# Optimization experiments

Hardware: AMD Instinct MI355X
Metric: run time of the kernel (lower is better)

Reference implementation:

```python
import jax, jax.numpy as jnp
import numpy as np

BETA = 1.0  # lagr_softmax default inverse temperature

def setup_inputs() -> dict:
    key = jax.random.key(0)
    ks = jax.random.split(key, 5)
    B, Tq, Tk, Eq, Ek, E, H = 2, 2048, 2048, 1024, 1024, 1024, 16
    s = lambda d: 1.0 / np.sqrt(d)
    return {
        "gq": jax.random.normal(ks[0], (B, Tq, Eq), jnp.float32),
        "gk": jax.random.normal(ks[1], (B, Tk, Ek), jnp.float32),
        "WQ": jax.random.normal(ks[2], (E, Eq), jnp.float32) * s(Eq),
        "WK": jax.random.normal(ks[3], (E, Ek), jnp.float32) * s(Ek),
        "Wmix": jax.random.normal(ks[4], (1, H), jnp.float32) * s(H),
    }

def reference(gq, gk, WQ, WK, Wmix):
    B, Tq, _ = gq.shape
    H = Wmix.shape[1]
    E = WQ.shape[0]
    D = E // H
    # Linear projections (bias=False): x @ W.T
    q = (gq @ WQ.T).reshape(B, Tq, H, D)          # (B,Tq,H,D)
    k = (gk @ WK.T).reshape(B, -1, H, D)          # (B,Tk,H,D)
    # scores q @ k^T per head: (B,H,Tq,Tk)
    a = jnp.einsum('bqhd,bkhd->bhqk', q, k)
    # mix_heads: Linear(n_heads -> 1) applied over head axis
    a = jnp.einsum('bhqk,h->bqk', a, Wmix[0])     # (B,Tq,Tk)
    # lagr_softmax: (1/beta) * logsumexp(beta * a, dim=-1)
    out = jax.nn.logsumexp(BETA * a, axis=-1) / BETA  # (B,Tq)
    return out[:, None, :]                        # (B,1,Tq) matching torch shape
```

## Files before the change

kernel.cpp:

```cpp
#include <hip/hip_runtime.h>
#include <hip/hip_bf16.h>
#include <math.h>

#define B_    2
#define TQ    2048
#define TK    2048
#define E_    1024
#define MTOT  4096

typedef __attribute__((ext_vector_type(8))) short bf16x8;
typedef __attribute__((ext_vector_type(4))) float f32x4;

__device__ __forceinline__ unsigned short f2bf(float x) {
  unsigned int u = __float_as_uint(x);
  u += 0x7fff + ((u >> 16) & 1);
  return (unsigned short)(u >> 16);
}

__device__ __forceinline__ void load_lds16(const void* g, void* l) {
  __builtin_amdgcn_global_load_lds(
      (const __attribute__((address_space(1))) unsigned int*)g,
      (__attribute__((address_space(3))) unsigned int*)l, 16, 0, 0);
}

#define BARRIER() do { asm volatile("" ::: "memory"); __builtin_amdgcn_s_barrier(); asm volatile("" ::: "memory"); } while (0)
#define WAIT_VM8()   do { asm volatile("s_waitcnt vmcnt(8)" ::: "memory"); __builtin_amdgcn_sched_barrier(0); } while (0)
#define WAIT_VM0()   do { asm volatile("s_waitcnt vmcnt(0)" ::: "memory"); __builtin_amdgcn_sched_barrier(0); } while (0)
#define WAIT_LGKM0() do { asm volatile("s_waitcnt lgkmcnt(0)" ::: "memory"); __builtin_amdgcn_sched_barrier(0); } while (0)


__device__ __forceinline__ void stage_tile(const unsigned short* gsrc, unsigned short* lds,
                                           int tid, int kt) {
  const int r  = tid >> 3;
  const int c8 = ((tid & 7) ^ (r & 7)) * 8;
  const unsigned short* g = gsrc + (size_t)r * E_ + (size_t)kt * 64 + c8;
  unsigned short* l = lds + tid * 8;
#pragma unroll
  for (int i = 0; i < 4; ++i)
    load_lds16(g + (size_t)(32 * i) * E_, l + 2048 * i);
}

#define LDS_AT(base, row, o) ((const bf16x8*)((base) + (((row) * 128 + ((o) ^ (((row) & 7) << 4))) >> 1)))

#define READ_ALL()                                                            \
  do {                                                                        \
    _Pragma("unroll") for (int f = 0; f < 4; ++f)                             \
      _Pragma("unroll") for (int ks = 0; ks < 2; ++ks) {                      \
        a[f][ks] = *LDS_AT(Ac, wm * 64 + f * 16 + li16, ks * 64 + hi4 * 16);  \
        b[f][ks] = *LDS_AT(Bc, wn * 64 + f * 16 + li16, ks * 64 + hi4 * 16);  \
      }                                                                       \
  } while (0)

#define MFMA_ALL()                                                            \
  do {                                                                        \
    __builtin_amdgcn_s_setprio(1);                                            \
    _Pragma("unroll") for (int ks = 0; ks < 2; ++ks)                          \
      _Pragma("unroll") for (int f = 0; f < 4; ++f)                           \
        _Pragma("unroll") for (int g = 0; g < 4; ++g)                         \
          acc[f][g] = __builtin_amdgcn_mfma_f32_16x16x32_bf16(                \
              a[f][ks], b[g][ks], acc[f][g], 0, 0, 0);                        \
    __builtin_amdgcn_s_setprio(0);                                            \
  } while (0)

#define GEMM_PIPELINE()                                                       \
  do {                                                                        \
    stage_tile(Ag, As[0], tid, 0); stage_tile(Bg, Bs[0], tid, 0);             \
    stage_tile(Ag, As[1], tid, 1); stage_tile(Bg, Bs[1], tid, 1);             \
    WAIT_VM8();                                                               \
    BARRIER();                                                                \
    for (int t = 0; t < 16; ++t) {                                            \
      const int c = t & 1;                                                    \
      unsigned short* Ac = As[c];                                             \
      unsigned short* Bc = Bs[c];                                             \
      READ_ALL();                                                             \
      WAIT_LGKM0();                     \
      BARRIER();                            \
      stage_tile(Ag, As[c], tid, (t + 2) & 15);                               \
      stage_tile(Bg, Bs[c], tid, (t + 2) & 15);                               \
      MFMA_ALL();                       \
      WAIT_VM8();                     \
      BARRIER();                                                              \
    }                                                                         \
  } while (0)

__global__ void prep_kernel(const float* __restrict__ gq, const float* __restrict__ gk,
                            const float* __restrict__ WQ, const float* __restrict__ WK,
                            const float* __restrict__ Wmix,
                            unsigned short* __restrict__ gqb, unsigned short* __restrict__ gkb,
                            unsigned short* __restrict__ wqb, unsigned short* __restrict__ wkb) {
  const int NGQ = (B_ * TQ * E_) / 4;
  const int NW  = (E_ * E_) / 4;
  const int total = 2 * NGQ + 2 * NW;
  for (int idx = blockIdx.x * blockDim.x + threadIdx.x; idx < total;
       idx += gridDim.x * blockDim.x) {
    const float4* src; unsigned short* dst; int local; float scale = 1.0f;
    if (idx < NGQ)            { src = (const float4*)gq; dst = gqb; local = idx; }
    else if (idx < 2 * NGQ)   { src = (const float4*)gk; dst = gkb; local = idx - NGQ; }
    else if (idx < 2*NGQ+NW)  { src = (const float4*)WQ; dst = wqb; local = idx - 2*NGQ;
                                scale = Wmix[local >> 14]; }
    else                      { src = (const float4*)WK; dst = wkb; local = idx - 2*NGQ - NW; }
    float4 v = src[local];
    ushort4 o;
    o.x = f2bf(v.x * scale); o.y = f2bf(v.y * scale);
    o.z = f2bf(v.z * scale); o.w = f2bf(v.w * scale);
    ((ushort4*)dst)[local] = o;
  }
}

__global__ __launch_bounds__(256, 2) void proj_kernel(
    const unsigned short* __restrict__ gqb, const unsigned short* __restrict__ gkb,
    const unsigned short* __restrict__ wqb, const unsigned short* __restrict__ wkb,
    unsigned short* __restrict__ qp, unsigned short* __restrict__ kp) {
  __shared__ __align__(16) unsigned short As[2][8192];
  __shared__ __align__(16) unsigned short Bs[2][8192];
  const int m0 = blockIdx.y * 128, n0 = blockIdx.x * 128;
  const unsigned short* Ag = (blockIdx.z ? gkb : gqb) + (size_t)m0 * E_;
  const unsigned short* Bg = (blockIdx.z ? wkb : wqb) + (size_t)n0 * E_;
  unsigned short* C        = (blockIdx.z ? kp  : qp);
  const int tid = threadIdx.x, wave = tid >> 6, lane = tid & 63;
  const int wm = wave >> 1, wn = wave & 1, li16 = lane & 15, hi4 = lane >> 4;
  f32x4 acc[4][4] = {};
  bf16x8 a[4][2];
  bf16x8 b[4][2];
  GEMM_PIPELINE();
#pragma unroll
  for (int f = 0; f < 4; ++f)
#pragma unroll
    for (int g = 0; g < 4; ++g)
#pragma unroll
      for (int j = 0; j < 4; ++j) {
        int row = m0 + wm * 64 + f * 16 + hi4 * 4 + j;
        int col = n0 + wn * 64 + g * 16 + li16;
        C[(size_t)row * E_ + col] = f2bf(acc[f][g][j]);
      }
  WAIT_VM0();
}

__global__ __launch_bounds__(256, 2) void score_lse_kernel(
    const unsigned short* __restrict__ qp, const unsigned short* __restrict__ kp,
    float2* __restrict__ partials) {
  __shared__ __align__(16) unsigned short As[2][8192];
  __shared__ __align__(16) unsigned short Bs[2][8192];
  __shared__ float redM[2][128];
  __shared__ float redS[2][128];
  const int bb = blockIdx.z;
  const int m0 = blockIdx.y * 128, n0 = blockIdx.x * 128;
  const unsigned short* Ag = qp + (size_t)bb * TQ * E_ + (size_t)m0 * E_;
  const unsigned short* Bg = kp + (size_t)bb * TK * E_ + (size_t)n0 * E_;
  const int tid = threadIdx.x, wave = tid >> 6, lane = tid & 63;
  const int wm = wave >> 1, wn = wave & 1, li16 = lane & 15, hi4 = lane >> 4;
  f32x4 acc[4][4] = {};
  bf16x8 a[4][2];
  bf16x8 b[4][2];
  GEMM_PIPELINE();
#pragma unroll
  for (int f = 0; f < 4; ++f) {
#pragma unroll
    for (int j = 0; j < 4; ++j) {
      float m = fmaxf(fmaxf(acc[f][0][j], acc[f][1][j]),
                      fmaxf(acc[f][2][j], acc[f][3][j]));
#pragma unroll
      for (int msk = 1; msk < 16; msk <<= 1) m = fmaxf(m, __shfl_xor(m, msk, 64));
      float s = 0.f;
#pragma unroll
      for (int g = 0; g < 4; ++g) s += expf(acc[f][g][j] - m);
#pragma unroll
      for (int msk = 1; msk < 16; msk <<= 1) s += __shfl_xor(s, msk, 64);
      if (li16 == 0) {
        int row = wm * 64 + f * 16 + hi4 * 4 + j;
        redM[wn][row] = m;
        redS[wn][row] = s;
      }
    }
  }
  __syncthreads();
  if (tid < 128) {
    float mA = redM[0][tid], mB = redM[1][tid];
    float M = fmaxf(mA, mB);
    float S = redS[0][tid] * expf(mA - M) + redS[1][tid] * expf(mB - M);
    int qrow = bb * TQ + m0 + tid;
    partials[(size_t)qrow * 16 + blockIdx.x] = make_float2(M, S);
  }
}

__global__ void finalize_kernel(const float2* __restrict__ partials, float* __restrict__ out) {
  int r = blockIdx.x * blockDim.x + threadIdx.x;
  if (r >= MTOT) return;
  const float2* p = partials + (size_t)r * 16;
  float M = p[0].x;
#pragma unroll
  for (int i = 1; i < 16; ++i) M = fmaxf(M, p[i].x);
  float S = 0.f;
#pragma unroll
  for (int i = 0; i < 16; ++i) S += p[i].y * expf(p[i].x - M);
  out[r] = logf(S) + M;
}

extern "C" void kernel_launch(void* const* d_in, const int* in_sizes, int n_in,
                              void* d_out, int out_size, void* d_ws, size_t ws_size,
                              hipStream_t stream) {
  const float* gq   = (const float*)d_in[0];
  const float* gk   = (const float*)d_in[1];
  const float* WQ   = (const float*)d_in[2];
  const float* WK   = (const float*)d_in[3];
  const float* Wmix = (const float*)d_in[4];
  float* out = (float*)d_out;

  char* ws = (char*)d_ws;
  unsigned short* gqb = (unsigned short*)(ws);
  unsigned short* gkb = (unsigned short*)(ws + 8388608);
  unsigned short* wqb = (unsigned short*)(ws + 16777216);
  unsigned short* wkb = (unsigned short*)(ws + 18874368);
  unsigned short* qp  = (unsigned short*)(ws + 20971520);
  unsigned short* kp  = (unsigned short*)(ws + 29360128);
  float2* partials    = (float2*)(ws + 37748736);

  hipLaunchKernelGGL(prep_kernel, dim3(1024), dim3(256), 0, stream,
                     gq, gk, WQ, WK, Wmix, gqb, gkb, wqb, wkb);
  hipLaunchKernelGGL(proj_kernel, dim3(8, 32, 2), dim3(256), 0, stream,
                     gqb, gkb, wqb, wkb, qp, kp);
  hipLaunchKernelGGL(score_lse_kernel, dim3(16, 16, 2), dim3(256), 0, stream,
                     qp, kp, partials);
  hipLaunchKernelGGL(finalize_kernel, dim3(16), dim3(256), 0, stream,
                     partials, out);
}
```

Before: 137.9 us.

## Enlarge GEMM tiles to 256x128 with 8 waves and triple-buffered A pipeline

Both GEMM kernels (projection and score/LSE) move from 128x128 tiles with 256 threads to 256x128 tiles with 512 threads. A is triple-buffered and B double-buffered in LDS. Each K step now uses a single barrier, with MFMA split into two halves so the global-to-LDS staging of B and A sits between them. The aim is to raise data reuse per B tile, cut barrier and wait overhead, and overlap loads with math more finely. In exchange, LDS use rises to about 128KB per block, which likely limits occupancy to one block per CU, and the grid shrinks to fewer blocks.

```diff
diff --git a/kernel.cpp b/kernel.cpp
--- a/kernel.cpp
+++ b/kernel.cpp
@@ -24,39 +24,53 @@
 }
 
 #define BARRIER() do { asm volatile("" ::: "memory"); __builtin_amdgcn_s_barrier(); asm volatile("" ::: "memory"); } while (0)
-#define WAIT_VM8()   do { asm volatile("s_waitcnt vmcnt(8)" ::: "memory"); __builtin_amdgcn_sched_barrier(0); } while (0)
-#define WAIT_VM0()   do { asm volatile("s_waitcnt vmcnt(0)" ::: "memory"); __builtin_amdgcn_sched_barrier(0); } while (0)
-#define WAIT_LGKM0() do { asm volatile("s_waitcnt lgkmcnt(0)" ::: "memory"); __builtin_amdgcn_sched_barrier(0); } while (0)
-
-
-__device__ __forceinline__ void stage_tile(const unsigned short* gsrc, unsigned short* lds,
-                                           int tid, int kt) {
+#define WAIT_VM4()   asm volatile("s_waitcnt vmcnt(4)" ::: "memory")
+#define WAIT_VM0()   asm volatile("s_waitcnt vmcnt(0)" ::: "memory")
+
+
+__device__ __forceinline__ void stage_A(const unsigned short* gsrc, unsigned short* lds,
+                                        int tid, int kt) {
   const int r  = tid >> 3;
   const int c8 = ((tid & 7) ^ (r & 7)) * 8;
   const unsigned short* g = gsrc + (size_t)r * E_ + (size_t)kt * 64 + c8;
   unsigned short* l = lds + tid * 8;
 #pragma unroll
   for (int i = 0; i < 4; ++i)
-    load_lds16(g + (size_t)(32 * i) * E_, l + 2048 * i);
+    load_lds16(g + (size_t)(64 * i) * E_, l + 4096 * i);
+}
+__device__ __forceinline__ void stage_B(const unsigned short* gsrc, unsigned short* lds,
+                                        int tid, int kt) {
+  const int r  = tid >> 3;
+  const int c8 = ((tid & 7) ^ (r & 7)) * 8;
+  const unsigned short* g = gsrc + (size_t)r * E_ + (size_t)kt * 64 + c8;
+  unsigned short* l = lds + tid * 8;
+#pragma unroll
+  for (int i = 0; i < 2; ++i)
+    load_lds16(g + (size_t)(64 * i) * E_, l + 4096 * i);
 }
 
 #define LDS_AT(base, row, o) ((const bf16x8*)((base) + (((row) * 128 + ((o) ^ (((row) & 7) << 4))) >> 1)))
 
-#define READ_ALL()                                                            \
+#define READ_A_ALL()                                                          \
   do {                                                                        \
     _Pragma("unroll") for (int f = 0; f < 4; ++f)                             \
-      _Pragma("unroll") for (int ks = 0; ks < 2; ++ks) {                      \
+      _Pragma("unroll") for (int ks = 0; ks < 2; ++ks)                        \
         a[f][ks] = *LDS_AT(Ac, wm * 64 + f * 16 + li16, ks * 64 + hi4 * 16);  \
-        b[f][ks] = *LDS_AT(Bc, wn * 64 + f * 16 + li16, ks * 64 + hi4 * 16);  \
-      }                                                                       \
-  } while (0)
-
-#define MFMA_ALL()                                                            \
+  } while (0)
+
+#define READ_B(g0)                                                            \
+  do {                                                                        \
+    _Pragma("unroll") for (int g = (g0); g < (g0) + 2; ++g)                   \
+      _Pragma("unroll") for (int ks = 0; ks < 2; ++ks)                        \
+        b[g][ks] = *LDS_AT(Bc, wn * 64 + g * 16 + li16, ks * 64 + hi4 * 16);  \
+  } while (0)
+
+#define MFMA_HALF(g0)                                                         \
   do {                                                                        \
     __builtin_amdgcn_s_setprio(1);                                            \
     _Pragma("unroll") for (int ks = 0; ks < 2; ++ks)                          \
       _Pragma("unroll") for (int f = 0; f < 4; ++f)                           \
-        _Pragma("unroll") for (int g = 0; g < 4; ++g)                         \
+        _Pragma("unroll") for (int g = (g0); g < (g0) + 2; ++g)               \
           acc[f][g] = __builtin_amdgcn_mfma_f32_16x16x32_bf16(                \
               a[f][ks], b[g][ks], acc[f][g], 0, 0, 0);                        \
     __builtin_amdgcn_s_setprio(0);                                            \
@@ -64,22 +78,26 @@
 
 #define GEMM_PIPELINE()                                                       \
   do {                                                                        \
-    stage_tile(Ag, As[0], tid, 0); stage_tile(Bg, Bs[0], tid, 0);             \
-    stage_tile(Ag, As[1], tid, 1); stage_tile(Bg, Bs[1], tid, 1);             \
-    WAIT_VM8();                                                               \
-    BARRIER();                                                                \
+    stage_A(Ag, Asl[0], tid, 0);                                              \
+    stage_B(Bg, Bsl[0], tid, 0);                                              \
+    stage_A(Ag, Asl[1], tid, 1);                                              \
+    WAIT_VM4();                   \
+    int s0 = 0, s2 = 2;                                     \
     for (int t = 0; t < 16; ++t) {                                            \
-      const int c = t & 1;                                                    \
-      unsigned short* Ac = As[c];                                             \
-      unsigned short* Bc = Bs[c];                                             \
-      READ_ALL();                                                             \
-      WAIT_LGKM0();                     \
-      BARRIER();                            \
-      stage_tile(Ag, As[c], tid, (t + 2) & 15);                               \
-      stage_tile(Bg, Bs[c], tid, (t + 2) & 15);                               \
-      MFMA_ALL();                       \
-      WAIT_VM8();                     \
       BARRIER();                                                              \
+      const unsigned short* Ac = Asl[s0];                                     \
+      const unsigned short* Bc = Bsl[t & 1];                                  \
+                                                         \
+      READ_A_ALL(); READ_B(0);                                                \
+      stage_B(Bg, Bsl[(t + 1) & 1], tid, (t + 1) & 15);                       \
+      MFMA_HALF(0);                                                           \
+                                                        \
+      READ_B(2);                                                              \
+      stage_A(Ag, Asl[s2], tid, (t + 2) & 15);                                \
+      MFMA_HALF(2);                                                           \
+      WAIT_VM4();                                                             \
+      s0 = (s0 == 2) ? 0 : s0 + 1;                                            \
+      s2 = (s2 == 2) ? 0 : s2 + 1;                                            \
     }                                                                         \
   } while (0)
 
@@ -107,13 +125,13 @@
   }
 }
 
-__global__ __launch_bounds__(256, 2) void proj_kernel(
+__global__ __launch_bounds__(512, 2) void proj_kernel(
     const unsigned short* __restrict__ gqb, const unsigned short* __restrict__ gkb,
     const unsigned short* __restrict__ wqb, const unsigned short* __restrict__ wkb,
     unsigned short* __restrict__ qp, unsigned short* __restrict__ kp) {
-  __shared__ __align__(16) unsigned short As[2][8192];
-  __shared__ __align__(16) unsigned short Bs[2][8192];
-  const int m0 = blockIdx.y * 128, n0 = blockIdx.x * 128;
+  __shared__ __align__(16) unsigned short Asl[3][16384];
+  __shared__ __align__(16) unsigned short Bsl[2][8192];
+  const int m0 = blockIdx.y * 256, n0 = blockIdx.x * 128;
   const unsigned short* Ag = (blockIdx.z ? gkb : gqb) + (size_t)m0 * E_;
   const unsigned short* Bg = (blockIdx.z ? wkb : wqb) + (size_t)n0 * E_;
   unsigned short* C        = (blockIdx.z ? kp  : qp);
@@ -136,15 +154,15 @@
   WAIT_VM0();
 }
 
-__global__ __launch_bounds__(256, 2) void score_lse_kernel(
+__global__ __launch_bounds__(512, 2) void score_lse_kernel(
     const unsigned short* __restrict__ qp, const unsigned short* __restrict__ kp,
     float2* __restrict__ partials) {
-  __shared__ __align__(16) unsigned short As[2][8192];
-  __shared__ __align__(16) unsigned short Bs[2][8192];
-  __shared__ float redM[2][128];
-  __shared__ float redS[2][128];
+  __shared__ __align__(16) unsigned short Asl[3][16384];
+  __shared__ __align__(16) unsigned short Bsl[2][8192];
+  __shared__ float redM[2][256];
+  __shared__ float redS[2][256];
   const int bb = blockIdx.z;
-  const int m0 = blockIdx.y * 128, n0 = blockIdx.x * 128;
+  const int m0 = blockIdx.y * 256, n0 = blockIdx.x * 128;
   const unsigned short* Ag = qp + (size_t)bb * TQ * E_ + (size_t)m0 * E_;
   const unsigned short* Bg = kp + (size_t)bb * TK * E_ + (size_t)n0 * E_;
   const int tid = threadIdx.x, wave = tid >> 6, lane = tid & 63;
@@ -174,7 +192,7 @@
     }
   }
   __syncthreads();
-  if (tid < 128) {
+  if (tid < 256) {
     float mA = redM[0][tid], mB = redM[1][tid];
     float M = fmaxf(mA, mB);
     float S = redS[0][tid] * expf(mA - M) + redS[1][tid] * expf(mB - M);
@@ -217,9 +235,9 @@
 
   hipLaunchKernelGGL(prep_kernel, dim3(1024), dim3(256), 0, stream,
                      gq, gk, WQ, WK, Wmix, gqb, gkb, wqb, wkb);
-  hipLaunchKernelGGL(proj_kernel, dim3(8, 32, 2), dim3(256), 0, stream,
+  hipLaunchKernelGGL(proj_kernel, dim3(8, 16, 2), dim3(512), 0, stream,
                      gqb, gkb, wqb, wkb, qp, kp);
-  hipLaunchKernelGGL(score_lse_kernel, dim3(16, 16, 2), dim3(256), 0, stream,
+  hipLaunchKernelGGL(score_lse_kernel, dim3(16, 8, 2), dim3(512), 0, stream,
                      qp, kp, partials);
   hipLaunchKernelGGL(finalize_kernel, dim3(16), dim3(256), 0, stream,
                      partials, out);
```

After: 142.2 us. 1.03x slower.
